# Optimization experiments

Hardware: AMD Instinct MI355X
Metric: run time of the kernel (lower is better)

## Reference

```python
import jax, jax.numpy as jnp
import numpy as np

B, T, D, H = 4, 2048, 1024, 16
Dh = D // H  # 64


def setup_inputs() -> dict:
    key = jax.random.key(0)
    ks = jax.random.split(key, 12)
    s = 1.0 / np.sqrt(D)
    return {
        "q": jax.random.normal(ks[0], (B, T, D), jnp.float32),
        "k": jax.random.normal(ks[1], (B, T, D), jnp.float32),
        "v": jax.random.normal(ks[2], (B, T, D), jnp.float32),
        "Wq": jax.random.normal(ks[3], (D, D), jnp.float32) * s,
        "bq": jnp.zeros((D,), jnp.float32),
        "Wk": jax.random.normal(ks[4], (D, D), jnp.float32) * s,
        "bk": jnp.zeros((D,), jnp.float32),
        "Wv": jax.random.normal(ks[5], (Dh, D), jnp.float32) * s,
        "bv": jnp.zeros((Dh,), jnp.float32),
        "Wo": jax.random.normal(ks[6], (D, D), jnp.float32) * s,
        "bo": jnp.zeros((D,), jnp.float32),
    }


def reference(q, k, v, Wq, bq, Wk, bk, Wv, bv, Wo, bo):
    # Projections (torch Linear: y = x @ W.T + b)
    Q = (q @ Wq.T + bq).reshape(B, T, H, Dh)   # [B,T,H,Dh]
    K = (k @ Wk.T + bk).reshape(B, T, H, Dh)   # [B,T,H,Dh]
    Vs = v @ Wv.T + bv                         # [B,T,Dh] shared across heads
    scale = 1.0 / np.sqrt(Dh).astype(np.float32)
    scores = jnp.einsum('bqhd,bkhd->bhqk', Q, K) * scale  # [B,H,T,T]
    attn = jax.nn.softmax(scores, axis=-1)
    # shared-V: broadcast V over heads
    out = jnp.einsum('bhqk,bkd->bqhd', attn, Vs)  # [B,T,H,Dh]
    out = out.reshape(B, T, D)
    y = out @ Wo.T + bo                           # [B,T,D]
    return y, attn.mean(axis=1)                   # per-head-averaged attention
```

## Files before the change

### kernel.cpp

```cpp
#include <hip/hip_runtime.h>
#include <cstdint>
#include <cstddef>

typedef __attribute__((ext_vector_type(8))) _Float16 half8;
typedef __attribute__((ext_vector_type(4))) _Float16 half4;
typedef __attribute__((ext_vector_type(4))) float f32x4;

#define DEV static __device__ __forceinline__
#define AS1(p) (const __attribute__((address_space(1))) void*)(p)
#define AS3(p) (__attribute__((address_space(3))) void*)(p)

#define LDS_BARRIER() asm volatile("s_waitcnt lgkmcnt(0)\n\ts_barrier" ::: "memory")

DEV half8 cvt8(const float* p) {
    f32x4 a = *(const f32x4*)p;
    f32x4 b = *(const f32x4*)(p + 4);
    half8 o;
    o[0] = (_Float16)a[0]; o[1] = (_Float16)a[1];
    o[2] = (_Float16)a[2]; o[3] = (_Float16)a[3];
    o[4] = (_Float16)b[0]; o[5] = (_Float16)b[1];
    o[6] = (_Float16)b[2]; o[7] = (_Float16)b[3];
    return o;
}

__global__ __launch_bounds__(256)
void cvt5_kernel(const float* __restrict__ q, _Float16* __restrict__ oq,
                 const float* __restrict__ k, _Float16* __restrict__ ok,
                 const float* __restrict__ wq, _Float16* __restrict__ owq,
                 const float* __restrict__ wk, _Float16* __restrict__ owk,
                 const float* __restrict__ wo, _Float16* __restrict__ owo)
{
    const int NQ = 1048576, NW = 131072;
    const int total = 2 * NQ + 3 * NW;
    int i = blockIdx.x * 256 + threadIdx.x;
    int stride = gridDim.x * 256;
    for (; i < total; i += stride) {
        if (i < NQ)            ((half8*)oq)[i] = cvt8(q + (size_t)i * 8);
        else if (i < 2 * NQ)   ((half8*)ok)[i - NQ] = cvt8(k + (size_t)(i - NQ) * 8);
        else {
            int j = i - 2 * NQ;
            if (j < NW)        ((half8*)owq)[j] = cvt8(wq + (size_t)j * 8);
            else if (j < 2*NW) ((half8*)owk)[j - NW] = cvt8(wk + (size_t)(j - NW) * 8);
            else               ((half8*)owo)[j - 2*NW] = cvt8(wo + (size_t)(j - 2*NW) * 8);
        }
    }
}

__global__ __launch_bounds__(256)
void combine_kernel(const _Float16* __restrict__ a, const _Float16* __restrict__ b,
                    float* __restrict__ out, int n8)
{
    int i = blockIdx.x * 256 + threadIdx.x;
    int stride = gridDim.x * 256;
    for (; i < n8; i += stride) {
        half8 x = ((const half8*)a)[i];
        half8 y = ((const half8*)b)[i];
        f32x4 o0, o1;
#pragma unroll
        for (int j = 0; j < 4; j++) o0[j] = ((float)x[j] + (float)y[j]) * 0.0625f;
#pragma unroll
        for (int j = 0; j < 4; j++) o1[j] = ((float)x[j + 4] + (float)y[j + 4]) * 0.0625f;
        *(f32x4*)(out + (size_t)i * 8) = o0;
        *(f32x4*)(out + (size_t)i * 8 + 4) = o1;
    }
}

#define GEMM_BODY(A, B, bias, scale, Cout)                                        \
    __shared__ half8 As[2][512];                                                  \
    __shared__ half8 Bs[2][512];                                                  \
    const int tid = threadIdx.x, l = tid & 63, w = tid >> 6;                      \
    const int lr = l & 15, lh = l >> 4;                                           \
    const int wm0 = (w >> 1) * 64, wn0 = (w & 1) * 64;                            \
    const int bm0 = blockIdx.x * 128, bn0 = blockIdx.y * 128;                     \
    const int nsteps = K >> 5;                                                    \
    f32x4 acc[4][4] = {};                                                         \
    STAGE(0, 0);                                                                  \
    __syncthreads();                                                              \
    for (int t = 0; t < nsteps; t++) {                                            \
        int cur = t & 1;                                                          \
        if (t + 1 < nsteps) STAGE(cur ^ 1, t + 1);                                \
        half8 a[4], b[4];                                                         \
        _Pragma("unroll")                                                         \
        for (int m = 0; m < 4; m++) a[m] = As[cur][lh * 128 + wm0 + m * 16 + lr]; \
        _Pragma("unroll")                                                         \
        for (int n = 0; n < 4; n++) b[n] = Bs[cur][lh * 128 + wn0 + n * 16 + lr]; \
        _Pragma("unroll")                                                         \
        for (int m = 0; m < 4; m++)                                               \
            _Pragma("unroll")                                                     \
            for (int n = 0; n < 4; n++)                                           \
                acc[m][n] = __builtin_amdgcn_mfma_f32_16x16x32_f16(a[m], b[n], acc[m][n], 0, 0, 0); \
        __syncthreads();                                                          \
    }                                                                             \
    _Pragma("unroll")                                                             \
    for (int m = 0; m < 4; m++)                                                   \
        _Pragma("unroll")                                                         \
        for (int n = 0; n < 4; n++) {                                             \
            int row0 = bm0 + wm0 + m * 16 + lh * 4;                               \
            int col = bn0 + wn0 + n * 16 + lr;                                    \
            float bv = bias[col];                                                 \
            _Pragma("unroll")                                                     \
            for (int j = 0; j < 4; j++) {                                         \
                float val = (acc[m][n][j] + bv) * scale;                          \
                int row = row0 + j;                                               \
                if constexpr (OUT_F16)                                            \
                    ((_Float16*)Cout)[(size_t)row * N + col] = (_Float16)val;     \
                else                                                              \
                    ((float*)Cout)[(size_t)row * N + col] = val;                  \
            }                                                                     \
        }

#define STAGE(buf, t) do {                                                        \
        int k0 = (t) << 5;                                                        \
        _Pragma("unroll")                                                         \
        for (int q2 = 0; q2 < 2; q2++) {                                          \
            int r = q2 * 64 + l;                                                  \
            __builtin_amdgcn_global_load_lds(                                     \
                AS1(A + (size_t)(bm0 + r) * K + k0 + w * 8),                      \
                AS3(&As[buf][w * 128 + q2 * 64]), 16, 0, 0);                      \
            __builtin_amdgcn_global_load_lds(                                     \
                AS1(B + (size_t)(bn0 + r) * K + k0 + w * 8),                      \
                AS3(&Bs[buf][w * 128 + q2 * 64]), 16, 0, 0);                      \
        }                                                                         \
    } while (0)

template<bool OUT_F16>
__global__ __launch_bounds__(256, 2)
void gemm16(const _Float16* __restrict__ A, const _Float16* __restrict__ B,
            const float* __restrict__ bias, float scale, void* __restrict__ Cout,
            int M, int N, int K)
{
    GEMM_BODY(A, B, bias, scale, Cout)
}

template<bool OUT_F16>
__global__ __launch_bounds__(256, 2)
void gemm16_dual(const _Float16* __restrict__ A0, const _Float16* __restrict__ B0,
                 const float* __restrict__ bias0, float scale0, void* __restrict__ C0,
                 const _Float16* __restrict__ A1, const _Float16* __restrict__ B1,
                 const float* __restrict__ bias1, float scale1, void* __restrict__ C1,
                 int M, int N, int K)
{
    const _Float16* A = blockIdx.z ? A1 : A0;
    const _Float16* B = blockIdx.z ? B1 : B0;
    const float* bias = blockIdx.z ? bias1 : bias0;
    float scale = blockIdx.z ? scale1 : scale0;
    void* Cout = blockIdx.z ? C1 : C0;
    GEMM_BODY(A, B, bias, scale, Cout)
}
#undef STAGE

template<int BM, int BN, int WR, int WC>
__global__ __launch_bounds__(256, 2)
void gemm_vp(const float* __restrict__ Aptr, const float* __restrict__ Bw,
             const float* __restrict__ bias, _Float16* __restrict__ Cout, int M, int N, int K)
{
    constexpr int BK = 32;
    constexpr int WM = BM / WR, WN = BN / WC;
    constexpr int MF = WM / 16, NF = WN / 16;
    constexpr int LDT = 40;
    __shared__ _Float16 Asl[BM][LDT];
    __shared__ _Float16 Bsl[BN][LDT];

    const int tid = threadIdx.x;
    const int l = tid & 63;
    const int w = tid >> 6;
    const int wr = w / WC, wc = w % WC;
    const int lr = l & 15, lh = l >> 4;
    const int bm0 = blockIdx.y * BM, bn0 = blockIdx.x * BN;

    f32x4 acc[MF][NF] = {};

    for (int k0 = 0; k0 < K; k0 += BK) {
        __syncthreads();
        for (int c = tid; c < BM * 4; c += 256) {
            int row = c >> 2, c8 = (c & 3) << 3;
            *(half8*)&Asl[row][c8] = cvt8(Aptr + (size_t)(bm0 + row) * K + k0 + c8);
        }
        for (int c = tid; c < BN * 4; c += 256) {
            int row = c >> 2, c8 = (c & 3) << 3;
            *(half8*)&Bsl[row][c8] = cvt8(Bw + (size_t)(bn0 + row) * K + k0 + c8);
        }
        __syncthreads();

        half8 a[MF], b[NF];
#pragma unroll
        for (int m = 0; m < MF; m++)
            a[m] = *(const half8*)&Asl[wr * WM + m * 16 + lr][lh * 8];
#pragma unroll
        for (int n = 0; n < NF; n++)
            b[n] = *(const half8*)&Bsl[wc * WN + n * 16 + lr][lh * 8];
#pragma unroll
        for (int m = 0; m < MF; m++)
#pragma unroll
            for (int n = 0; n < NF; n++)
                acc[m][n] = __builtin_amdgcn_mfma_f32_16x16x32_f16(a[m], b[n], acc[m][n], 0, 0, 0);
    }

#pragma unroll
    for (int m = 0; m < MF; m++)
#pragma unroll
        for (int n = 0; n < NF; n++) {
            int row0 = bm0 + wr * WM + m * 16 + lh * 4;
            int col = bn0 + wc * WN + n * 16 + lr;
            float bv = bias[col];
#pragma unroll
            for (int j = 0; j < 4; j++) {
                float val = acc[m][n][j] + bv;
                int row = row0 + j;
                int bi = row >> 11, t = row & 2047;
                Cout[(((size_t)(bi * 64 + col)) << 11) + t] = (_Float16)val;
            }
        }
}

#define LK(dst, kt) do {                                                          \
        const _Float16* kp_ = Kb + (size_t)((kt) * 32) * 1024;                    \
        _Pragma("unroll")                                                         \
        for (int kfr_ = 0; kfr_ < 2; kfr_++)                                      \
            _Pragma("unroll")                                                     \
            for (int dk_ = 0; dk_ < 2; dk_++)                                     \
                dst[kfr_][dk_] = *(const half8*)(kp_ + (size_t)(kfr_ * 16 + lr) * 1024 \
                                                 + ch + dk_ * 32 + lh * 8);       \
    } while (0)

__global__ __launch_bounds__(512, 4)
void attn_fused(const _Float16* __restrict__ Qh, const _Float16* __restrict__ Kh,
                const _Float16* __restrict__ VT, _Float16* __restrict__ attnp,
                _Float16* __restrict__ Op)
{
    const int blk = blockIdx.x;
    const int b = blk & 3;
    const int hg = (blk >> 2) & 1;
    const int q0 = (blk >> 3) << 5;
    const int tid = threadIdx.x;
    const int l = tid & 63, w = tid >> 6;
    const int lr = l & 15, lh = l >> 4;
    const int ch = (hg * 8 + w) * 64;

    __shared__ __align__(16) _Float16 Pld[2][8][32][40];

    const size_t base = (size_t)b * 2048 * 1024;
    const _Float16* Qb = Qh + base;
    const _Float16* Kb = Kh + base;

    half8 qf[2][2];
#pragma unroll
    for (int m = 0; m < 2; m++)
#pragma unroll
        for (int dk = 0; dk < 2; dk++)
            qf[m][dk] = *(const half8*)(Qb + (size_t)(q0 + m * 16 + lr) * 1024
                                        + ch + dk * 32 + lh * 8);

    float sl[2][4] = {};
    {
        half8 ka[2][2], kb2[2][2];
#define SBODY(KF) do {                                                            \
        f32x4 sc[2][2] = {};                                                      \
        _Pragma("unroll")                                                         \
        for (int m = 0; m < 2; m++)                                               \
            _Pragma("unroll")                                                     \
            for (int kfr = 0; kfr < 2; kfr++)                                     \
                _Pragma("unroll")                                                 \
                for (int dk = 0; dk < 2; dk++)                                    \
                    sc[m][kfr] = __builtin_amdgcn_mfma_f32_16x16x32_f16(          \
                        qf[m][dk], KF[kfr][dk], sc[m][kfr], 0, 0, 0);             \
        _Pragma("unroll")                                                         \
        for (int m = 0; m < 2; m++)                                               \
            _Pragma("unroll")                                                     \
            for (int j = 0; j < 4; j++)                                           \
                sl[m][j] += __builtin_amdgcn_exp2f(sc[m][0][j])                   \
                          + __builtin_amdgcn_exp2f(sc[m][1][j]);                  \
    } while (0)
        LK(ka, 0);
        for (int kt = 0; kt < 64; kt += 2) {
            LK(kb2, kt + 1);
            SBODY(ka);
            LK(ka, kt + 2 < 64 ? kt + 2 : 63);
            SBODY(kb2);
        }
#undef SBODY
    }
#pragma unroll
    for (int m = 0; m < 2; m++)
#pragma unroll
        for (int j = 0; j < 4; j++) {
            float s = sl[m][j];
#pragma unroll
            for (int d = 1; d < 16; d <<= 1)
                s += __shfl_xor(s, d, 64);
            sl[m][j] = s;
        }
    float rinv[2];
#pragma unroll
    for (int m = 0; m < 2; m++) {
        int src = (lr >> 2) << 4;
        float t0 = __shfl(sl[m][0], src, 64);
        float t1 = __shfl(sl[m][1], src, 64);
        float t2 = __shfl(sl[m][2], src, 64);
        float t3 = __shfl(sl[m][3], src, 64);
        int jj = lr & 3;
        float s = (jj == 0) ? t0 : (jj == 1) ? t1 : (jj == 2) ? t2 : t3;
        rinv[m] = 1.0f / s;
    }

    f32x4 oacc[2][4] = {};
    half8 ka[2][2], kb2[2][2];

#define EBODY(KF, KT, P) do {                                                     \
        const int krow = (KT) * 32;                                               \
        f32x4 sc[2][2] = {};                                                      \
        _Pragma("unroll")                                                         \
        for (int m = 0; m < 2; m++)                                               \
            _Pragma("unroll")                                                     \
            for (int kfr = 0; kfr < 2; kfr++)                                     \
                _Pragma("unroll")                                                 \
                for (int dk = 0; dk < 2; dk++)                                    \
                    sc[m][kfr] = __builtin_amdgcn_mfma_f32_16x16x32_f16(          \
                        KF[kfr][dk], qf[m][dk], sc[m][kfr], 0, 0, 0);             \
        _Pragma("unroll")                                                         \
        for (int m = 0; m < 2; m++)                                               \
            _Pragma("unroll")                                                     \
            for (int kfr = 0; kfr < 2; kfr++) {                                   \
                half4 pk4;                                                        \
                _Pragma("unroll")                                                 \
                for (int j = 0; j < 4; j++)                                       \
                    pk4[j] = (_Float16)(__builtin_amdgcn_exp2f(sc[m][kfr][j])     \
                                        * rinv[m]);                               \
                *(half4*)&Pld[P][w][m * 16 + lr][kfr * 16 + lh * 4] = pk4;        \
            }                                                                     \
        half8 vf[4], pa[2];                                                       \
        _Pragma("unroll")                                                         \
        for (int dv = 0; dv < 4; dv++)                                            \
            vf[dv] = *(const half8*)(VT + (((size_t)(b * 64 + dv * 16 + lr)) << 11) + krow + lh * 8); \
        _Pragma("unroll")                                                         \
        for (int m = 0; m < 2; m++)                                               \
            pa[m] = *(const half8*)&Pld[P][w][m * 16 + lr][lh * 8];               \
        _Pragma("unroll")                                                         \
        for (int m = 0; m < 2; m++)                                               \
            _Pragma("unroll")                                                     \
            for (int dv = 0; dv < 4; dv++)                                        \
                oacc[m][dv] = __builtin_amdgcn_mfma_f32_16x16x32_f16(             \
                    pa[m], vf[dv], oacc[m][dv], 0, 0, 0);                         \
        LDS_BARRIER();                                                            \
        {                                                                         \
            int r = tid >> 4, c2 = (tid & 15) * 2;                                \
            float s0 = 0.f, s1 = 0.f;                                             \
            _Pragma("unroll")                                                     \
            for (int ww = 0; ww < 8; ww++) {                                      \
                union { uint32_t u; _Float16 h[2]; } pv;                          \
                pv.u = *(const uint32_t*)&Pld[P][ww][r][c2];                      \
                s0 += (float)pv.h[0]; s1 += (float)pv.h[1];                       \
            }                                                                     \
            union { _Float16 h[2]; uint32_t u; } pk;                              \
            pk.h[0] = (_Float16)s0; pk.h[1] = (_Float16)s1;                       \
            __builtin_nontemporal_store(pk.u, (uint32_t*)(attnp                   \
                + (size_t)hg * 16777216 + (((size_t)(b * 2048 + q0 + r)) << 11)   \
                + krow + c2));                                                    \
        }                                                                         \
    } while (0)

    LK(ka, 0);
    for (int i = 0; i < 64; i += 2) {
        LK(kb2, i + 1);
        EBODY(ka, i, 0);
        LK(ka, i + 2 < 64 ? i + 2 : 63);
        EBODY(kb2, i + 1, 1);
    }
#undef EBODY

    _Float16* op = Op + base;
#pragma unroll
    for (int m = 0; m < 2; m++)
#pragma unroll
        for (int dv = 0; dv < 4; dv++)
#pragma unroll
            for (int j = 0; j < 4; j++) {
                int row = q0 + m * 16 + lh * 4 + j;
                int col = ch + dv * 16 + lr;
                op[(size_t)row * 1024 + col] = (_Float16)oacc[m][dv][j];
            }
}

extern "C" void kernel_launch(void* const* d_in, const int* in_sizes, int n_in,
                              void* d_out, int out_size, void* d_ws, size_t ws_size,
                              hipStream_t stream)
{
    const float* q  = (const float*)d_in[0];
    const float* k  = (const float*)d_in[1];
    const float* v  = (const float*)d_in[2];
    const float* Wq = (const float*)d_in[3];
    const float* bq = (const float*)d_in[4];
    const float* Wk = (const float*)d_in[5];
    const float* bk = (const float*)d_in[6];
    const float* Wv = (const float*)d_in[7];
    const float* bv = (const float*)d_in[8];
    const float* Wo = (const float*)d_in[9];
    const float* bo = (const float*)d_in[10];

    float* y = (float*)d_out;
    float* attn_mean = y + (size_t)4 * 2048 * 1024;

    uint8_t* ws = (uint8_t*)d_ws;
    _Float16* Qh  = (_Float16*)(ws);
    _Float16* Kh  = (_Float16*)(ws + 16777216);
    _Float16* VT  = (_Float16*)(ws + 33554432);
    _Float16* Wqc = (_Float16*)(ws + 34603008);
    _Float16* Wkc = (_Float16*)(ws + 36700160);
    _Float16* Woc = (_Float16*)(ws + 38797312);
    _Float16* qc  = (_Float16*)(ws + 40894464);
    _Float16* kc  = (_Float16*)(ws + 57671680);
    _Float16* Op  = qc;
    _Float16* attnp = (_Float16*)(ws + 74448896);

    const float QS = 0.125f * 1.44269504088896340736f;

    cvt5_kernel<<<dim3(2048), dim3(256), 0, stream>>>(q, qc, k, kc, Wq, Wqc, Wk, Wkc, Wo, Woc);

    gemm16_dual<true><<<dim3(64, 8, 2), dim3(256), 0, stream>>>(
        qc, Wqc, bq, QS, Qh, kc, Wkc, bk, 1.0f, Kh, 8192, 1024, 1024);
    gemm_vp<64, 64, 2, 2><<<dim3(1, 128), dim3(256), 0, stream>>>(v, Wv, bv, VT, 8192, 64, 1024);

    attn_fused<<<dim3(512), dim3(512), 0, stream>>>(Qh, Kh, VT, attnp, Op);

    combine_kernel<<<dim3(2048), dim3(256), 0, stream>>>(
        attnp, attnp + (size_t)16777216, attn_mean, 2097152);

    gemm16<false><<<dim3(64, 8), dim3(256), 0, stream>>>(Op, Woc, bo, 1.0f, y, 8192, 1024, 1024);
}
```

Before: 532.3 us.

## Merge V projection into conversion kernel and combine into output GEMM

The V projection GEMM now runs in its own block range inside the fp32-to-fp16 conversion kernel. The attention-mean combine now runs in its own block range inside the output projection GEMM. This cuts the launch count from six to four and lets independent work share the GPU at the same time, so small kernels no longer leave the machine underused. The risk is uneven block mixes, for example the 128 V-projection blocks running long next to the conversion blocks, and higher LDS use in the merged kernels.

```diff
diff --git a/kernel.cpp b/kernel.cpp
--- a/kernel.cpp
+++ b/kernel.cpp
@@ -23,91 +23,89 @@
     return o;
 }
 
-__global__ __launch_bounds__(256)
-void cvt5_kernel(const float* __restrict__ q, _Float16* __restrict__ oq,
+__global__ __launch_bounds__(256, 2)
+void prep_kernel(const float* __restrict__ v, const float* __restrict__ Wv,
+                 const float* __restrict__ bv, _Float16* __restrict__ VT,
+                 const float* __restrict__ q, _Float16* __restrict__ oq,
                  const float* __restrict__ k, _Float16* __restrict__ ok,
                  const float* __restrict__ wq, _Float16* __restrict__ owq,
                  const float* __restrict__ wk, _Float16* __restrict__ owk,
                  const float* __restrict__ wo, _Float16* __restrict__ owo)
 {
-    const int NQ = 1048576, NW = 131072;
-    const int total = 2 * NQ + 3 * NW;
-    int i = blockIdx.x * 256 + threadIdx.x;
-    int stride = gridDim.x * 256;
-    for (; i < total; i += stride) {
-        if (i < NQ)            ((half8*)oq)[i] = cvt8(q + (size_t)i * 8);
-        else if (i < 2 * NQ)   ((half8*)ok)[i - NQ] = cvt8(k + (size_t)(i - NQ) * 8);
-        else {
-            int j = i - 2 * NQ;
-            if (j < NW)        ((half8*)owq)[j] = cvt8(wq + (size_t)j * 8);
-            else if (j < 2*NW) ((half8*)owk)[j - NW] = cvt8(wk + (size_t)(j - NW) * 8);
-            else               ((half8*)owo)[j - 2*NW] = cvt8(wo + (size_t)(j - 2*NW) * 8);
+    __shared__ _Float16 Asl[64][40];
+    __shared__ _Float16 Bsl[64][40];
+
+    if (blockIdx.x < 128) {
+        const int tid = threadIdx.x;
+        const int l = tid & 63, w = tid >> 6;
+        const int wr = w >> 1, wc = w & 1;
+        const int lr = l & 15, lh = l >> 4;
+        const int bm0 = blockIdx.x * 64;
+        const int K = 1024;
+
+        f32x4 acc[2][2] = {};
+
+        for (int k0 = 0; k0 < K; k0 += 32) {
+            __syncthreads();
+            for (int c = tid; c < 256; c += 256) {
+                int row = c >> 2, c8 = (c & 3) << 3;
+                *(half8*)&Asl[row][c8] = cvt8(v + (size_t)(bm0 + row) * K + k0 + c8);
+            }
+            {
+                int c = tid;
+                if (c < 256) {
+                    int row = c >> 2, c8 = (c & 3) << 3;
+                    *(half8*)&Bsl[row][c8] = cvt8(Wv + (size_t)row * K + k0 + c8);
+                }
+            }
+            __syncthreads();
+
+            half8 a[2], b[2];
+#pragma unroll
+            for (int m = 0; m < 2; m++)
+                a[m] = *(const half8*)&Asl[wr * 32 + m * 16 + lr][lh * 8];
+#pragma unroll
+            for (int n = 0; n < 2; n++)
+                b[n] = *(const half8*)&Bsl[wc * 32 + n * 16 + lr][lh * 8];
+#pragma unroll
+            for (int m = 0; m < 2; m++)
+#pragma unroll
+                for (int n = 0; n < 2; n++)
+                    acc[m][n] = __builtin_amdgcn_mfma_f32_16x16x32_f16(a[m], b[n], acc[m][n], 0, 0, 0);
+        }
+
+#pragma unroll
+        for (int m = 0; m < 2; m++)
+#pragma unroll
+            for (int n = 0; n < 2; n++) {
+                int row0 = bm0 + wr * 32 + m * 16 + lh * 4;
+                int col = wc * 32 + n * 16 + lr;
+                float bvv = bv[col];
+#pragma unroll
+                for (int j = 0; j < 4; j++) {
+                    float val = acc[m][n][j] + bvv;
+                    int row = row0 + j;
+                    int bi = row >> 11, t = row & 2047;
+                    VT[(((size_t)(bi * 64 + col)) << 11) + t] = (_Float16)val;
+                }
+            }
+    } else {
+        const int NQ = 1048576, NW = 131072;
+        const int total = 2 * NQ + 3 * NW;
+        int i = (blockIdx.x - 128) * 256 + threadIdx.x;
+        int stride = 2048 * 256;
+        for (; i < total; i += stride) {
+            if (i < NQ)            ((half8*)oq)[i] = cvt8(q + (size_t)i * 8);
+            else if (i < 2 * NQ)   ((half8*)ok)[i - NQ] = cvt8(k + (size_t)(i - NQ) * 8);
+            else {
+                int j = i - 2 * NQ;
+                if (j < NW)        ((half8*)owq)[j] = cvt8(wq + (size_t)j * 8);
+                else if (j < 2*NW) ((half8*)owk)[j - NW] = cvt8(wk + (size_t)(j - NW) * 8);
+                else               ((half8*)owo)[j - 2*NW] = cvt8(wo + (size_t)(j - 2*NW) * 8);
+            }
         }
     }
 }
-
-__global__ __launch_bounds__(256)
-void combine_kernel(const _Float16* __restrict__ a, const _Float16* __restrict__ b,
-                    float* __restrict__ out, int n8)
-{
-    int i = blockIdx.x * 256 + threadIdx.x;
-    int stride = gridDim.x * 256;
-    for (; i < n8; i += stride) {
-        half8 x = ((const half8*)a)[i];
-        half8 y = ((const half8*)b)[i];
-        f32x4 o0, o1;
-#pragma unroll
-        for (int j = 0; j < 4; j++) o0[j] = ((float)x[j] + (float)y[j]) * 0.0625f;
-#pragma unroll
-        for (int j = 0; j < 4; j++) o1[j] = ((float)x[j + 4] + (float)y[j + 4]) * 0.0625f;
-        *(f32x4*)(out + (size_t)i * 8) = o0;
-        *(f32x4*)(out + (size_t)i * 8 + 4) = o1;
-    }
-}
-
-#define GEMM_BODY(A, B, bias, scale, Cout)                                        \
-    __shared__ half8 As[2][512];                                                  \
-    __shared__ half8 Bs[2][512];                                                  \
-    const int tid = threadIdx.x, l = tid & 63, w = tid >> 6;                      \
-    const int lr = l & 15, lh = l >> 4;                                           \
-    const int wm0 = (w >> 1) * 64, wn0 = (w & 1) * 64;                            \
-    const int bm0 = blockIdx.x * 128, bn0 = blockIdx.y * 128;                     \
-    const int nsteps = K >> 5;                                                    \
-    f32x4 acc[4][4] = {};                                                         \
-    STAGE(0, 0);                                                                  \
-    __syncthreads();                                                              \
-    for (int t = 0; t < nsteps; t++) {                                            \
-        int cur = t & 1;                                                          \
-        if (t + 1 < nsteps) STAGE(cur ^ 1, t + 1);                                \
-        half8 a[4], b[4];                                                         \
-        _Pragma("unroll")                                                         \
-        for (int m = 0; m < 4; m++) a[m] = As[cur][lh * 128 + wm0 + m * 16 + lr]; \
-        _Pragma("unroll")                                                         \
-        for (int n = 0; n < 4; n++) b[n] = Bs[cur][lh * 128 + wn0 + n * 16 + lr]; \
-        _Pragma("unroll")                                                         \
-        for (int m = 0; m < 4; m++)                                               \
-            _Pragma("unroll")                                                     \
-            for (int n = 0; n < 4; n++)                                           \
-                acc[m][n] = __builtin_amdgcn_mfma_f32_16x16x32_f16(a[m], b[n], acc[m][n], 0, 0, 0); \
-        __syncthreads();                                                          \
-    }                                                                             \
-    _Pragma("unroll")                                                             \
-    for (int m = 0; m < 4; m++)                                                   \
-        _Pragma("unroll")                                                         \
-        for (int n = 0; n < 4; n++) {                                             \
-            int row0 = bm0 + wm0 + m * 16 + lh * 4;                               \
-            int col = bn0 + wn0 + n * 16 + lr;                                    \
-            float bv = bias[col];                                                 \
-            _Pragma("unroll")                                                     \
-            for (int j = 0; j < 4; j++) {                                         \
-                float val = (acc[m][n][j] + bv) * scale;                          \
-                int row = row0 + j;                                               \
-                if constexpr (OUT_F16)                                            \
-                    ((_Float16*)Cout)[(size_t)row * N + col] = (_Float16)val;     \
-                else                                                              \
-                    ((float*)Cout)[(size_t)row * N + col] = val;                  \
-            }                                                                     \
-        }
 
 #define STAGE(buf, t) do {                                                        \
         int k0 = (t) << 5;                                                        \
@@ -123,95 +121,93 @@
         }                                                                         \
     } while (0)
 
-template<bool OUT_F16>
-__global__ __launch_bounds__(256, 2)
-void gemm16(const _Float16* __restrict__ A, const _Float16* __restrict__ B,
-            const float* __restrict__ bias, float scale, void* __restrict__ Cout,
-            int M, int N, int K)
-{
-    GEMM_BODY(A, B, bias, scale, Cout)
-}
-
-template<bool OUT_F16>
+#define GEMM_CORE(BM0, BN0, OUTSTMT)                                              \
+    const int tid = threadIdx.x, l = tid & 63, w = tid >> 6;                      \
+    const int lr = l & 15, lh = l >> 4;                                           \
+    const int wm0 = (w >> 1) * 64, wn0 = (w & 1) * 64;                            \
+    const int bm0 = (BM0), bn0 = (BN0);                                           \
+    const int nsteps = K >> 5;                                                    \
+    f32x4 acc[4][4] = {};                                                         \
+    STAGE(0, 0);                                                                  \
+    __syncthreads();                                                              \
+    for (int t = 0; t < nsteps; t++) {                                            \
+        int cur = t & 1;                                                          \
+        if (t + 1 < nsteps) STAGE(cur ^ 1, t + 1);                                \
+        half8 a[4], b[4];                                                         \
+        _Pragma("unroll")                                                         \
+        for (int m = 0; m < 4; m++) a[m] = As[cur][lh * 128 + wm0 + m * 16 + lr]; \
+        _Pragma("unroll")                                                         \
+        for (int n = 0; n < 4; n++) b[n] = Bs[cur][lh * 128 + wn0 + n * 16 + lr]; \
+        _Pragma("unroll")                                                         \
+        for (int m = 0; m < 4; m++)                                               \
+            _Pragma("unroll")                                                     \
+            for (int n = 0; n < 4; n++)                                           \
+                acc[m][n] = __builtin_amdgcn_mfma_f32_16x16x32_f16(a[m], b[n], acc[m][n], 0, 0, 0); \
+        __syncthreads();                                                          \
+    }                                                                             \
+    _Pragma("unroll")                                                             \
+    for (int m = 0; m < 4; m++)                                                   \
+        _Pragma("unroll")                                                         \
+        for (int n = 0; n < 4; n++) {                                             \
+            int row0 = bm0 + wm0 + m * 16 + lh * 4;                               \
+            int col = bn0 + wn0 + n * 16 + lr;                                    \
+            float bvv = bias[col];                                                \
+            _Pragma("unroll")                                                     \
+            for (int j = 0; j < 4; j++) {                                         \
+                float val = (acc[m][n][j] + bvv) * scale;                         \
+                int row = row0 + j;                                               \
+                OUTSTMT;                                                          \
+            }                                                                     \
+        }
+
 __global__ __launch_bounds__(256, 2)
 void gemm16_dual(const _Float16* __restrict__ A0, const _Float16* __restrict__ B0,
-                 const float* __restrict__ bias0, float scale0, void* __restrict__ C0,
+                 const float* __restrict__ bias0, float scale0, _Float16* __restrict__ C0,
                  const _Float16* __restrict__ A1, const _Float16* __restrict__ B1,
-                 const float* __restrict__ bias1, float scale1, void* __restrict__ C1,
+                 const float* __restrict__ bias1, float scale1, _Float16* __restrict__ C1,
                  int M, int N, int K)
 {
+    __shared__ half8 As[2][512];
+    __shared__ half8 Bs[2][512];
     const _Float16* A = blockIdx.z ? A1 : A0;
     const _Float16* B = blockIdx.z ? B1 : B0;
     const float* bias = blockIdx.z ? bias1 : bias0;
     float scale = blockIdx.z ? scale1 : scale0;
-    void* Cout = blockIdx.z ? C1 : C0;
-    GEMM_BODY(A, B, bias, scale, Cout)
+    _Float16* Cout = blockIdx.z ? C1 : C0;
+    GEMM_CORE(blockIdx.x * 128, blockIdx.y * 128,
+              Cout[(size_t)row * N + col] = (_Float16)val)
+}
+
+__global__ __launch_bounds__(256, 2)
+void ygc_kernel(const _Float16* __restrict__ A, const _Float16* __restrict__ B,
+                const float* __restrict__ bias, float scale, float* __restrict__ Cout,
+                int M, int N, int K,
+                const _Float16* __restrict__ p0, const _Float16* __restrict__ p1,
+                float* __restrict__ amean, int n8)
+{
+    __shared__ half8 As[2][512];
+    __shared__ half8 Bs[2][512];
+    if (blockIdx.x < 512) {
+        const int bid = blockIdx.x;
+        GEMM_CORE((bid & 63) * 128, (bid >> 6) * 128,
+                  Cout[(size_t)row * N + col] = val)
+    } else {
+        int i = (blockIdx.x - 512) * 256 + threadIdx.x;
+        int stride = 512 * 256;
+        for (; i < n8; i += stride) {
+            half8 x = ((const half8*)p0)[i];
+            half8 y = ((const half8*)p1)[i];
+            f32x4 o0, o1;
+#pragma unroll
+            for (int j = 0; j < 4; j++) o0[j] = ((float)x[j] + (float)y[j]) * 0.0625f;
+#pragma unroll
+            for (int j = 0; j < 4; j++) o1[j] = ((float)x[j + 4] + (float)y[j + 4]) * 0.0625f;
+            *(f32x4*)(amean + (size_t)i * 8) = o0;
+            *(f32x4*)(amean + (size_t)i * 8 + 4) = o1;
+        }
+    }
 }
 #undef STAGE
-
-template<int BM, int BN, int WR, int WC>
-__global__ __launch_bounds__(256, 2)
-void gemm_vp(const float* __restrict__ Aptr, const float* __restrict__ Bw,
-             const float* __restrict__ bias, _Float16* __restrict__ Cout, int M, int N, int K)
-{
-    constexpr int BK = 32;
-    constexpr int WM = BM / WR, WN = BN / WC;
-    constexpr int MF = WM / 16, NF = WN / 16;
-    constexpr int LDT = 40;
-    __shared__ _Float16 Asl[BM][LDT];
-    __shared__ _Float16 Bsl[BN][LDT];
-
-    const int tid = threadIdx.x;
-    const int l = tid & 63;
-    const int w = tid >> 6;
-    const int wr = w / WC, wc = w % WC;
-    const int lr = l & 15, lh = l >> 4;
-    const int bm0 = blockIdx.y * BM, bn0 = blockIdx.x * BN;
-
-    f32x4 acc[MF][NF] = {};
-
-    for (int k0 = 0; k0 < K; k0 += BK) {
-        __syncthreads();
-        for (int c = tid; c < BM * 4; c += 256) {
-            int row = c >> 2, c8 = (c & 3) << 3;
-            *(half8*)&Asl[row][c8] = cvt8(Aptr + (size_t)(bm0 + row) * K + k0 + c8);
-        }
-        for (int c = tid; c < BN * 4; c += 256) {
-            int row = c >> 2, c8 = (c & 3) << 3;
-            *(half8*)&Bsl[row][c8] = cvt8(Bw + (size_t)(bn0 + row) * K + k0 + c8);
-        }
-        __syncthreads();
-
-        half8 a[MF], b[NF];
-#pragma unroll
-        for (int m = 0; m < MF; m++)
-            a[m] = *(const half8*)&Asl[wr * WM + m * 16 + lr][lh * 8];
-#pragma unroll
-        for (int n = 0; n < NF; n++)
-            b[n] = *(const half8*)&Bsl[wc * WN + n * 16 + lr][lh * 8];
-#pragma unroll
-        for (int m = 0; m < MF; m++)
-#pragma unroll
-            for (int n = 0; n < NF; n++)
-                acc[m][n] = __builtin_amdgcn_mfma_f32_16x16x32_f16(a[m], b[n], acc[m][n], 0, 0, 0);
-    }
-
-#pragma unroll
-    for (int m = 0; m < MF; m++)
-#pragma unroll
-        for (int n = 0; n < NF; n++) {
-            int row0 = bm0 + wr * WM + m * 16 + lh * 4;
-            int col = bn0 + wc * WN + n * 16 + lr;
-            float bv = bias[col];
-#pragma unroll
-            for (int j = 0; j < 4; j++) {
-                float val = acc[m][n][j] + bv;
-                int row = row0 + j;
-                int bi = row >> 11, t = row & 2047;
-                Cout[(((size_t)(bi * 64 + col)) << 11) + t] = (_Float16)val;
-            }
-        }
-}
 
 #define LK(dst, kt) do {                                                          \
         const _Float16* kp_ = Kb + (size_t)((kt) * 32) * 1024;                    \
@@ -221,6 +217,24 @@
             for (int dk_ = 0; dk_ < 2; dk_++)                                     \
                 dst[kfr_][dk_] = *(const half8*)(kp_ + (size_t)(kfr_ * 16 + lr) * 1024 \
                                                  + ch + dk_ * 32 + lh * 8);       \
+    } while (0)
+
+#define SBODY(KF) do {                                                            \
+        f32x4 sc[2][2] = {};                                                      \
+        _Pragma("unroll")                                                         \
+        for (int m = 0; m < 2; m++)                                               \
+            _Pragma("unroll")                                                     \
+            for (int kfr = 0; kfr < 2; kfr++)                                     \
+                _Pragma("unroll")                                                 \
+                for (int dk = 0; dk < 2; dk++)                                    \
+                    sc[m][kfr] = __builtin_amdgcn_mfma_f32_16x16x32_f16(          \
+                        qf[m][dk], KF[kfr][dk], sc[m][kfr], 0, 0, 0);             \
+        _Pragma("unroll")                                                         \
+        for (int m = 0; m < 2; m++)                                               \
+            _Pragma("unroll")                                                     \
+            for (int j = 0; j < 4; j++)                                           \
+                sl[m][j] += __builtin_amdgcn_exp2f(sc[m][0][j])                   \
+                          + __builtin_amdgcn_exp2f(sc[m][1][j]);                  \
     } while (0)
 
 __global__ __launch_bounds__(512, 4)
@@ -254,23 +268,6 @@
     float sl[2][4] = {};
     {
         half8 ka[2][2], kb2[2][2];
-#define SBODY(KF) do {                                                            \
-        f32x4 sc[2][2] = {};                                                      \
-        _Pragma("unroll")                                                         \
-        for (int m = 0; m < 2; m++)                                               \
-            _Pragma("unroll")                                                     \
-            for (int kfr = 0; kfr < 2; kfr++)                                     \
-                _Pragma("unroll")                                                 \
-                for (int dk = 0; dk < 2; dk++)                                    \
-                    sc[m][kfr] = __builtin_amdgcn_mfma_f32_16x16x32_f16(          \
-                        qf[m][dk], KF[kfr][dk], sc[m][kfr], 0, 0, 0);             \
-        _Pragma("unroll")                                                         \
-        for (int m = 0; m < 2; m++)                                               \
-            _Pragma("unroll")                                                     \
-            for (int j = 0; j < 4; j++)                                           \
-                sl[m][j] += __builtin_amdgcn_exp2f(sc[m][0][j])                   \
-                          + __builtin_amdgcn_exp2f(sc[m][1][j]);                  \
-    } while (0)
         LK(ka, 0);
         for (int kt = 0; kt < 64; kt += 2) {
             LK(kb2, kt + 1);
@@ -278,7 +275,6 @@
             LK(ka, kt + 2 < 64 ? kt + 2 : 63);
             SBODY(kb2);
         }
-#undef SBODY
     }
 #pragma unroll
     for (int m = 0; m < 2; m++)
@@ -414,16 +410,15 @@
 
     const float QS = 0.125f * 1.44269504088896340736f;
 
-    cvt5_kernel<<<dim3(2048), dim3(256), 0, stream>>>(q, qc, k, kc, Wq, Wqc, Wk, Wkc, Wo, Woc);
-
-    gemm16_dual<true><<<dim3(64, 8, 2), dim3(256), 0, stream>>>(
+    prep_kernel<<<dim3(2176), dim3(256), 0, stream>>>(
+        v, Wv, bv, VT, q, qc, k, kc, Wq, Wqc, Wk, Wkc, Wo, Woc);
+
+    gemm16_dual<<<dim3(64, 8, 2), dim3(256), 0, stream>>>(
         qc, Wqc, bq, QS, Qh, kc, Wkc, bk, 1.0f, Kh, 8192, 1024, 1024);
-    gemm_vp<64, 64, 2, 2><<<dim3(1, 128), dim3(256), 0, stream>>>(v, Wv, bv, VT, 8192, 64, 1024);
 
     attn_fused<<<dim3(512), dim3(512), 0, stream>>>(Qh, Kh, VT, attnp, Op);
 
-    combine_kernel<<<dim3(2048), dim3(256), 0, stream>>>(
+    ygc_kernel<<<dim3(1024), dim3(256), 0, stream>>>(
+        Op, Woc, bo, 1.0f, y, 8192, 1024, 1024,
         attnp, attnp + (size_t)16777216, attn_mean, 2097152);
-
-    gemm16<false><<<dim3(64, 8), dim3(256), 0, stream>>>(Op, Woc, bo, 1.0f, y, 8192, 1024, 1024);
-}
+}
```

Result: faster. 512.9 us (median of 2 runs) (-3.6%).
